# Kernel optimization log

Hardware: AMD Instinct MI355X
Metric: run time of the kernel (lower is better)

## Reference

```python
import jax, jax.numpy as jnp
import numpy as np

B = 256
NUM_PRIMARY = 32      # cfg.num_primary_caps
PRIM_ATOMS = 8
NUM_CLASSES = 10
DIGIT_ATOMS = 16
NUM_ROUTING = 3       # cfg.num_routing (DigitCap)
IN_DIM = 6 * 6 * NUM_PRIMARY  # 1152
NUM_PIXELS = 28 * 28 * 1


def squash(s, axis):
    # v = ||s||^2/(1+||s||^2) * s/||s||
    n2 = jnp.sum(jnp.square(s), axis=axis, keepdims=True)
    return s * (n2 / (1.0 + n2)) / jnp.sqrt(n2 + 1e-9)


def conv2d(x, w, stride):
    return jax.lax.conv_general_dilated(
        x, w, (stride, stride), 'VALID',
        dimension_numbers=('NCHW', 'OIHW', 'NCHW'))


def setup_inputs() -> dict:
    key = jax.random.key(0)
    ks = jax.random.split(key, 10)
    x = jax.random.uniform(ks[0], (B, 1, 28, 28), jnp.float32)
    labels = jax.random.randint(ks[1], (B,), 0, NUM_CLASSES)
    y = jax.nn.one_hot(labels, NUM_CLASSES, dtype=jnp.float32)
    conv1_w = 0.05 * jax.random.normal(ks[2], (256, 1, 9, 9), jnp.float32)
    conv1_b = jnp.full((256,), 0.1, jnp.float32)
    # primary capsule conv: 256 -> 32 caps * 8 atoms, k=9, s=2 (bias applied after routing)
    prim_w = 0.05 * jax.random.normal(ks[3], (NUM_PRIMARY * PRIM_ATOMS, 256, 9, 9), jnp.float32)
    prim_b = jnp.full((NUM_PRIMARY, PRIM_ATOMS), 0.1, jnp.float32)
    # digit capsule transform: [in_dim, in_atoms, out_dim, out_atoms]
    digit_w = 0.05 * jax.random.normal(ks[4], (IN_DIM, PRIM_ATOMS, NUM_CLASSES, DIGIT_ATOMS), jnp.float32)
    digit_b = jnp.full((NUM_CLASSES, DIGIT_ATOMS), 0.1, jnp.float32)
    w1 = 0.05 * jax.random.normal(ks[5], (NUM_CLASSES * DIGIT_ATOMS, 512), jnp.float32)
    b1 = jnp.zeros((512,), jnp.float32)
    w2 = 0.05 * jax.random.normal(ks[6], (512, 1024), jnp.float32)
    b2 = jnp.zeros((1024,), jnp.float32)
    w3 = 0.05 * jax.random.normal(ks[7], (1024, NUM_PIXELS), jnp.float32)
    b3 = jnp.zeros((NUM_PIXELS,), jnp.float32)
    return dict(x=x, y=y, conv1_w=conv1_w, conv1_b=conv1_b, prim_w=prim_w,
                prim_b=prim_b, digit_w=digit_w, digit_b=digit_b,
                w1=w1, b1=b1, w2=w2, b2=b2, w3=w3, b3=b3)


def reference(x, y, conv1_w, conv1_b, prim_w, prim_b, digit_w, digit_b,
              w1, b1, w2, b2, w3, b3):
    # conv stem
    h = jax.nn.relu(conv2d(x, conv1_w, 1) + conv1_b[None, :, None, None])  # [B,256,20,20]

    # PrimaryCap: conv votes [B, in_dim=1, out=32, atoms=8, 6, 6]; num_routing=1
    votes_p = conv2d(h, prim_w, 2).reshape(B, NUM_PRIMARY, PRIM_ATOMS, 6, 6)
    # one routing iter, input_dim=1: softmax(zeros) over output_dim -> uniform 1/32
    preact_p = votes_p / NUM_PRIMARY + prim_b[None, :, :, None, None]
    caps1 = squash(preact_p, axis=2)  # [B,32,8,6,6]

    # permute(0,1,3,4,2) then flatten -> [B, 1152, 8]
    x3 = jnp.transpose(caps1, (0, 1, 3, 4, 2)).reshape(B, IN_DIM, PRIM_ATOMS)

    # DigitCap votes: [B, in_dim, out_dim, out_atoms]
    votes = jnp.einsum('bia,iaot->biot', x3, digit_w)
    logits = jnp.zeros((B, IN_DIM, NUM_CLASSES), votes.dtype)
    act = None
    for _ in range(NUM_ROUTING):
        route = jax.nn.softmax(logits, axis=2)  # over output capsules
        preact = jnp.einsum('bio,biot->bot', route, votes) + digit_b
        act = squash(preact, axis=-1)  # [B,10,16]
        logits = logits + jnp.einsum('biot,bot->bio', votes, act)
    digit = act

    # Reconstruction: mask by label, 160 -> 512 -> 1024 -> 784
    masked = (digit * y[:, :, None]).reshape(B, NUM_CLASSES * DIGIT_ATOMS)
    r = jax.nn.relu(masked @ w1 + b1)
    r = jax.nn.relu(r @ w2 + b2)
    recon = jax.nn.sigmoid(r @ w3 + b3)
    return digit, recon
```

## Files before the change

### kernel.cpp

```cpp
#include <hip/hip_runtime.h>
#include <hip/hip_bf16.h>

typedef unsigned short u16;
typedef unsigned int u32;

static __device__ __forceinline__ float us2f(u16 u) {
    return __uint_as_float(((u32)u) << 16);
}
static __device__ __forceinline__ u16 f2bu(float f) {
    u32 u = __float_as_uint(f);
    return (u16)((u + 0x7fffu + ((u >> 16) & 1u)) >> 16);
}

typedef __attribute__((ext_vector_type(8))) __bf16 bf16x8;
typedef __attribute__((ext_vector_type(4))) float f32x4;

static __device__ __forceinline__ void async16(const u16* g, u16* l) {
    __builtin_amdgcn_global_load_lds(
        (const __attribute__((address_space(1))) unsigned int*)g,
        (__attribute__((address_space(3))) unsigned int*)l, 16, 0, 0);
}

__global__ void fill_sentinel(float* out, int n, float val) {
    int g = blockIdx.x * 256 + threadIdx.x;
    if (g < n) out[g] = val;
}

__global__ __launch_bounds__(256) void prep1(const float* __restrict__ pw,
    u16* __restrict__ wt, float* __restrict__ x3m)
{
    __shared__ u16 wl[81 * 258];
    const int bid = blockIdx.x, tid = threadIdx.x;
    if (bid < 256) {
        const float* ws = pw + (size_t)bid * 20736;
        for (int idx = tid; idx < 20736; idx += 256) {
            const int cc = idx / 81, kk = idx - cc * 81;
            wl[kk * 258 + cc] = f2bu(ws[idx]);
        }
        __syncthreads();
        u16* wo = wt + (size_t)bid * 20736;
        for (int q = tid; q < 20736; q += 256)
            wo[q] = wl[(q >> 8) * 258 + (q & 255)];
    } else {
        float4 z = {0.f, 0.f, 0.f, 0.f};
        reinterpret_cast<float4*>(x3m)[(size_t)(bid - 256) * 256 + tid] = z;
    }
}

__global__ __launch_bounds__(256) void prep2(const float* __restrict__ dw,
    u16* __restrict__ dwb_t, float* __restrict__ preactD)
{
    const int bid = blockIdx.x, tid = threadIdx.x;
    if (bid < 5760) {
        const int g = bid * 256 + tid;
        dwb_t[g] = f2bu(dw[g]);
    } else {
        float4 z = {0.f, 0.f, 0.f, 0.f};
        reinterpret_cast<float4*>(preactD)[(size_t)(bid - 5760) * 256 + tid] = z;
    }
}

__global__ __launch_bounds__(256) void conv1_kernel(const float* __restrict__ x,
    const float* __restrict__ wfull, const float* __restrict__ bias, u16* __restrict__ h)
{
    __shared__ float xs[784];
    __shared__ u16 wl[81 * 256];
    const int b = blockIdx.x >> 2, g = blockIdx.x & 3;
    const int c = threadIdx.x;
    for (int idx = c; idx < 784; idx += 256) xs[idx] = x[b * 784 + idx];
    for (int idx = c; idx < 20736; idx += 256)
        wl[idx] = f2bu(wfull[(idx & 255) * 81 + (idx >> 8)]);
    __syncthreads();
    const float bv = bias[c];
    #pragma unroll 1
    for (int iy = g * 5; iy < g * 5 + 5; ++iy) {
        float acc[20];
        #pragma unroll
        for (int i = 0; i < 20; ++i) acc[i] = bv;
        #pragma unroll 1
        for (int dy = 0; dy < 9; ++dy) {
            float xr[28];
            const float4* xrow = reinterpret_cast<const float4*>(&xs[(iy + dy) * 28]);
            #pragma unroll
            for (int i = 0; i < 7; ++i) {
                float4 v = xrow[i];
                xr[4*i] = v.x; xr[4*i+1] = v.y; xr[4*i+2] = v.z; xr[4*i+3] = v.w;
            }
            #pragma unroll
            for (int dx = 0; dx < 9; ++dx) {
                const float wv = us2f(wl[(dy * 9 + dx) * 256 + c]);
                #pragma unroll
                for (int ix = 0; ix < 20; ++ix) acc[ix] += xr[ix + dx] * wv;
            }
        }
        u16* hp = h + ((b * 20 + iy) * 20) * 256 + c;
        #pragma unroll
        for (int ix = 0; ix < 20; ++ix) hp[ix * 256] = f2bu(fmaxf(acc[ix], 0.f));
    }
}

__global__ __launch_bounds__(256, 2) void prim_gemm_split(const u16* __restrict__ h,
    const u16* __restrict__ wT, float* __restrict__ pm)
{
    __shared__ u16 As[3 * 4096];
    __shared__ u16 Bs[3 * 8192];
    const int tid = threadIdx.x;
    const int split = blockIdx.y;
    const int mBase = blockIdx.x * 128;
    const int lane = tid & 63, wv = tid >> 6;
    const int swzq = (tid & 3) ^ ((lane >> 3) & 3);
    const int rA = wv * 32 + (lane >> 2);
    const int rB = wv * 64 + (lane >> 2);
    int mA0 = mBase + rA;
    int bA0 = mA0 / 36, rr0 = mA0 % 36;
    const int aBase0 = ((bA0 * 20 + 2 * (rr0 / 6)) * 20 + 2 * (rr0 % 6)) * 256 + swzq * 8;
    int mA1 = mA0 + 16;
    int bA1 = mA1 / 36, rr1 = mA1 % 36;
    const int aBase1 = ((bA1 * 20 + 2 * (rr1 / 6)) * 20 + 2 * (rr1 % 6)) * 256 + swzq * 8;
    const u16* bp0 = wT + (size_t)rB * 20736 + swzq * 8;

    int kglob = split * 3456;
    int ky = kglob / 2304; int krem = kglob - ky * 2304;
    int kx = krem >> 8; int c0 = krem & 255;

    f32x4 acc[4][8];
    #pragma unroll
    for (int i = 0; i < 4; ++i)
        #pragma unroll
        for (int j = 0; j < 8; ++j) acc[i][j] = (f32x4){0.f, 0.f, 0.f, 0.f};

    const int wm = wv >> 1, wn = wv & 1;
    const int lcol = lane & 15, lquad = lane >> 4;
    const int rswz = (lquad ^ ((lcol >> 1) & 3)) * 8;
    const u16* Arow = As + (wm * 64 + lcol) * 32 + rswz;
    const u16* Brow = Bs + (wn * 128 + lcol) * 32 + rswz;
    u16* aD = As + wv * 1024;
    u16* bD = Bs + wv * 2048;

    #define STAGE(sel)  do {                                                   \
        const int koffA = (ky * 20 + kx) * 256 + c0;                           \
        async16(h + aBase0 + koffA, aD + (sel) * 4096);                        \
        async16(h + aBase1 + koffA, aD + (sel) * 4096 + 512);                  \
        async16(bp0 + kglob,          bD + (sel) * 8192);                      \
        async16(bp0 + 331776 + kglob, bD + (sel) * 8192 + 512);               \
        async16(bp0 + 663552 + kglob, bD + (sel) * 8192 + 1024);              \
        async16(bp0 + 995328 + kglob, bD + (sel) * 8192 + 1536);              \
        kglob += 32; c0 += 32;                                                 \
        if (c0 == 256) { c0 = 0; if (++kx == 9) { kx = 0; ++ky; } }            \
    } while (0)

    #define COMPUTE(sel)  do {                                                 \
        const u16* Ab = Arow + (sel) * 4096;                                   \
        const u16* Bb = Brow + (sel) * 8192;                                   \
        bf16x8 af[4], bfr[8];                                                  \
        _Pragma("unroll")                                                      \
        for (int i = 0; i < 4; ++i)                                            \
            af[i] = *reinterpret_cast<const bf16x8*>(Ab + i * 512);            \
        _Pragma("unroll")                                                      \
        for (int j = 0; j < 8; ++j)                                            \
            bfr[j] = *reinterpret_cast<const bf16x8*>(Bb + j * 512);           \
        __builtin_amdgcn_s_setprio(1);                                         \
        _Pragma("unroll")                                                      \
        for (int i = 0; i < 4; ++i)                                            \
            _Pragma("unroll")                                                  \
            for (int j = 0; j < 8; ++j)                                        \
                acc[i][j] = __builtin_amdgcn_mfma_f32_16x16x32_bf16(af[i], bfr[j], acc[i][j], 0, 0, 0); \
        __builtin_amdgcn_s_setprio(0);                                         \
    } while (0)

    STAGE(0);
    STAGE(1);
    int cb = 0, sb = 2;
    #pragma unroll 1
    for (int kt = 0; kt < 106; ++kt) {
        STAGE(sb);
        asm volatile("s_waitcnt vmcnt(12)" ::: "memory");
        __builtin_amdgcn_s_barrier();
        __builtin_amdgcn_sched_barrier(0);
        COMPUTE(cb);
        __builtin_amdgcn_sched_barrier(0);
        __builtin_amdgcn_s_barrier();
        __builtin_amdgcn_sched_barrier(0);
        cb = (cb == 2) ? 0 : cb + 1;
        sb = (sb == 2) ? 0 : sb + 1;
    }
    asm volatile("s_waitcnt vmcnt(6)" ::: "memory");
    __builtin_amdgcn_s_barrier();
    __builtin_amdgcn_sched_barrier(0);
    COMPUTE(1);
    __builtin_amdgcn_sched_barrier(0);
    asm volatile("s_waitcnt vmcnt(0)" ::: "memory");
    __builtin_amdgcn_s_barrier();
    __builtin_amdgcn_sched_barrier(0);
    COMPUTE(2);
    #undef STAGE
    #undef COMPUTE

    #pragma unroll
    for (int i = 0; i < 4; ++i) {
        const int mrow = mBase + wm * 64 + i * 16 + lquad * 4;
        #pragma unroll
        for (int j = 0; j < 8; ++j) {
            const int ncol = wn * 128 + j * 16 + lcol;
            #pragma unroll
            for (int r = 0; r < 4; ++r)
                unsafeAtomicAdd(&pm[(size_t)(mrow + r) * 256 + ncol], acc[i][j][r]);
        }
    }
}

__global__ __launch_bounds__(192) void votes_gemm(const float* __restrict__ x3m,
    const float* __restrict__ pb, const u16* __restrict__ dwb_t,
    u16* __restrict__ votes, int hb)
{
    __shared__ float dws[8 * 1280];
    __shared__ float x3s[64 * 64];
    __shared__ float pbs[256];
    const int ic = blockIdx.x * 8, bc = blockIdx.y * 64;
    const int tid = threadIdx.x;
    for (int q = tid; q < 256; q += 192) pbs[q] = pb[q];
    for (int q = tid; q < 10240; q += 192)
        dws[q] = us2f(dwb_t[(size_t)ic * 1280 + q]);
    __syncthreads();
    for (int g = tid; g < 512; g += 192) {
        const int b_l = g >> 3, i_l = g & 7;
        const int i = ic + i_l, cap = i / 36, p = i - cap * 36;
        const float* src = &x3m[((size_t)(hb + bc + b_l) * 36 + p) * 256 + cap * 8];
        float v[8]; float n2 = 0.f;
        #pragma unroll
        for (int a = 0; a < 8; ++a) {
            v[a] = src[a] * (1.f / 32.f) + pbs[cap * 8 + a];
            n2 += v[a] * v[a];
        }
        const float scale = (n2 / (1.f + n2)) * rsqrtf(n2 + 1e-9f);
        #pragma unroll
        for (int a = 0; a < 8; ++a)
            x3s[b_l * 64 + i_l * 8 + a] = v[a] * scale;
    }
    __syncthreads();
    if (tid < 160) {
        const int ot = tid;
        float dwr[8][8];
        #pragma unroll
        for (int i_l = 0; i_l < 8; ++i_l)
            #pragma unroll
            for (int a = 0; a < 8; ++a)
                dwr[i_l][a] = dws[i_l * 1280 + a * 160 + ot];
        #pragma unroll 1
        for (int b_l = 0; b_l < 64; ++b_l) {
            u16 ob[8];
            #pragma unroll
            for (int i_l = 0; i_l < 8; ++i_l) {
                const float* xp = &x3s[b_l * 64 + i_l * 8];
                float v = 0.f;
                #pragma unroll
                for (int a = 0; a < 8; ++a) v += xp[a] * dwr[i_l][a];
                ob[i_l] = f2bu(v);
            }
            uint4 o4;
            o4.x = (u32)ob[0] | ((u32)ob[1] << 16);
            o4.y = (u32)ob[2] | ((u32)ob[3] << 16);
            o4.z = (u32)ob[4] | ((u32)ob[5] << 16);
            o4.w = (u32)ob[6] | ((u32)ob[7] << 16);
            *reinterpret_cast<uint4*>(&votes[((size_t)(bc + b_l) * 160 + ot) * 1152 + ic]) = o4;
        }
    }
}

__global__ __launch_bounds__(256) void routing_fused(const u16* __restrict__ votes,
    const float* __restrict__ pD_prev, const float* __restrict__ db,
    float* __restrict__ logits, float* __restrict__ pD_next, int hb, int mode)
{
    __shared__ u16 vs16[160 * 146];
    __shared__ float route_s[144 * 10];
    __shared__ float act_s[160];
    const int ic = blockIdx.x * 144, b_l = blockIdx.y, gb = hb + b_l;
    const int tid = threadIdx.x;

    for (int q = tid; q < 2880; q += 256) {
        const int ot = q / 18, ch = q - ot * 18;
        const uint4 d = *reinterpret_cast<const uint4*>(
            &votes[((size_t)b_l * 160 + ot) * 1152 + ic + ch * 8]);
        u32* vp = reinterpret_cast<u32*>(&vs16[ot * 146 + ch * 8]);
        vp[0] = d.x; vp[1] = d.y; vp[2] = d.z; vp[3] = d.w;
    }
    if (mode >= 1 && tid < 160) {
        float pre = pD_prev[(size_t)gb * 160 + tid] + db[tid];
        float sq = pre * pre;
        sq += __shfl_xor(sq, 1); sq += __shfl_xor(sq, 2);
        sq += __shfl_xor(sq, 4); sq += __shfl_xor(sq, 8);
        act_s[tid] = pre * (sq / (1.f + sq)) * rsqrtf(sq + 1e-9f);
    }
    __syncthreads();

    if (mode >= 1) {
        if (tid < 144) {
            float acc[10];
            #pragma unroll
            for (int k = 0; k < 10; ++k) acc[k] = 0.f;
            #pragma unroll 4
            for (int ot = 0; ot < 160; ++ot)
                acc[ot >> 4] += us2f(vs16[ot * 146 + tid]) * act_s[ot];
            float* lp = &logits[((size_t)gb * 1152 + ic + tid) * 10];
            float l[10];
            if (mode == 1) {
                #pragma unroll
                for (int k = 0; k < 10; ++k) { l[k] = acc[k]; lp[k] = l[k]; }
            } else {
                #pragma unroll
                for (int k = 0; k < 10; ++k) { l[k] = lp[k] + acc[k]; lp[k] = l[k]; }
            }
            float mx = -1e30f;
            #pragma unroll
            for (int k = 0; k < 10; ++k) mx = fmaxf(mx, l[k]);
            float s = 0.f;
            #pragma unroll
            for (int k = 0; k < 10; ++k) { l[k] = __expf(l[k] - mx); s += l[k]; }
            const float inv = 1.f / s;
            #pragma unroll
            for (int k = 0; k < 10; ++k) route_s[tid * 10 + k] = l[k] * inv;
        }
        __syncthreads();
    }

    if (tid < 160) {
        const int o = tid >> 4;
        const u16* vrow = &vs16[tid * 146];
        float acc2 = 0.f;
        if (mode == 0) {
            float s = 0.f;
            #pragma unroll 8
            for (int i = 0; i < 144; ++i) s += us2f(vrow[i]);
            acc2 = 0.1f * s;
        } else {
            const float* rp = &route_s[o];
            #pragma unroll 8
            for (int i = 0; i < 144; ++i)
                acc2 += rp[i * 10] * us2f(vrow[i]);
        }
        unsafeAtomicAdd(&pD_next[(size_t)gb * 160 + tid], acc2);
    }
}

__global__ __launch_bounds__(256) void mlp_layer(const float* __restrict__ in,
    const float* __restrict__ maskY, const float* __restrict__ w,
    const float* __restrict__ bias, float* __restrict__ outp, int K, int N, int mode,
    const float* __restrict__ db2, float* __restrict__ dout)
{
    __shared__ float ins[4 * 1024];
    __shared__ float scl[40];
    const int b0 = blockIdx.x * 4;
    const int n = blockIdx.y * 256 + threadIdx.x;
    if (db2) {
        if (threadIdx.x < 40) {
            const int b_l = threadIdx.x / 10, o = threadIdx.x - b_l * 10;
            const float* pp = &in[(size_t)(b0 + b_l) * 160 + o * 16];
            float n2 = 0.f;
            #pragma unroll
            for (int t = 0; t < 16; ++t) {
                float pv = pp[t] + db2[o * 16 + t];
                n2 += pv * pv;
            }
            scl[threadIdx.x] = (n2 / (1.f + n2)) * rsqrtf(n2 + 1e-9f);
        }
        __syncthreads();
        for (int idx = threadIdx.x; idx < 4 * 160; idx += 256) {
            const int b_l = idx / 160, j = idx - b_l * 160;
            float a = (in[(size_t)(b0 + b_l) * 160 + j] + db2[j]) * scl[b_l * 10 + (j >> 4)];
            if (blockIdx.y == 0 && dout) dout[(size_t)(b0 + b_l) * 160 + j] = a;
            ins[idx] = a * maskY[(b0 + b_l) * 10 + (j >> 4)];
        }
    } else {
        for (int idx = threadIdx.x; idx < 4 * K; idx += 256) {
            float v = in[(size_t)b0 * K + idx];
            if (maskY) {
                const int b_l = idx / K, j = idx % K;
                v *= maskY[(b0 + b_l) * 10 + (j >> 4)];
            }
            ins[idx] = v;
        }
    }
    __syncthreads();
    if (n < N) {
        float a0 = 0.f, a1 = 0.f, a2 = 0.f, a3 = 0.f;
        for (int k = 0; k < K; ++k) {
            const float wvv = w[(size_t)k * N + n];
            a0 += ins[k] * wvv;
            a1 += ins[K + k] * wvv;
            a2 += ins[2 * K + k] * wvv;
            a3 += ins[3 * K + k] * wvv;
        }
        const float bv = bias[n];
        float v[4] = {a0 + bv, a1 + bv, a2 + bv, a3 + bv};
        #pragma unroll
        for (int j = 0; j < 4; ++j) {
            float xv = v[j];
            xv = (mode == 0) ? fmaxf(xv, 0.f) : 1.f / (1.f + __expf(-xv));
            outp[(size_t)(b0 + j) * N + n] = xv;
        }
    }
}

extern "C" void kernel_launch(void* const* d_in, const int* in_sizes, int n_in,
                              void* d_out, int out_size, void* d_ws, size_t ws_size,
                              hipStream_t stream) {
    const float* x   = (const float*)d_in[0];
    const float* y   = (const float*)d_in[1];
    const float* c1w = (const float*)d_in[2];
    const float* c1b = (const float*)d_in[3];
    const float* pw  = (const float*)d_in[4];
    const float* pb  = (const float*)d_in[5];
    const float* dw  = (const float*)d_in[6];
    const float* db  = (const float*)d_in[7];
    const float* w1  = (const float*)d_in[8];
    const float* b1  = (const float*)d_in[9];
    const float* w2  = (const float*)d_in[10];
    const float* b2  = (const float*)d_in[11];
    const float* w3  = (const float*)d_in[12];
    const float* b3  = (const float*)d_in[13];
    float* out = (float*)d_out;
    char* ws = (char*)d_ws;

    static const int exp_sizes[14] = {200704, 2560, 20736, 256, 5308416, 256,
                                      1474560, 160, 81920, 512, 524288, 1024,
                                      802816, 784};
    int bad = (n_in == 14) ? -1 : -2;
    if (bad == -1)
        for (int i = 0; i < 14; ++i) if (in_sizes[i] != exp_sizes[i]) { bad = i; break; }
    if (bad != -1) {
        fill_sentinel<<<(out_size + 255) / 256, 256, 0, stream>>>(out, out_size,
            7168.f + 16.f * (float)(bad + 1));
        return;
    }
    const size_t NEEDED = 72482816ULL;
    if (ws_size < NEEDED) {
        fill_sentinel<<<(out_size + 255) / 256, 256, 0, stream>>>(out, out_size, 111.0f);
        return;
    }

    u16*   h       = (u16*)(ws);
    u16*   wT2     = (u16*)(ws + 52428800);
    float* x3m     = (float*)(ws + 63045632);
    u16*   votes   = (u16*)(ws);
    float* logits  = (float*)(ws + 47185920);
    float* preactD = (float*)(ws + 59146240);
    u16*   dwb_t   = (u16*)(ws + 59637760);
    float* r1      = (float*)(ws + 62586880);
    float* r2      = (float*)(ws + 63111168);

    prep1<<<2560, 256, 0, stream>>>(pw, wT2, x3m);
    conv1_kernel<<<1024, 256, 0, stream>>>(x, c1w, c1b, h);
    prim_gemm_split<<<dim3(72, 6), 256, 0, stream>>>(h, wT2, x3m);
    prep2<<<5880, 256, 0, stream>>>(dw, dwb_t, preactD);

    float* pD0 = preactD, *pD1 = preactD + 40960, *pD2 = preactD + 81920;
    for (int half = 0; half < 2; ++half) {
        const int hb = half * 128;
        votes_gemm<<<dim3(144, 2), 192, 0, stream>>>(x3m, pb, dwb_t, votes, hb);
        routing_fused<<<dim3(8, 128), 256, 0, stream>>>(votes, pD0, db, logits, pD0, hb, 0);
        routing_fused<<<dim3(8, 128), 256, 0, stream>>>(votes, pD0, db, logits, pD1, hb, 1);
        routing_fused<<<dim3(8, 128), 256, 0, stream>>>(votes, pD1, db, logits, pD2, hb, 2);
    }

    mlp_layer<<<dim3(64, 2), 256, 0, stream>>>(pD2, y, w1, b1, r1, 160, 512, 0, db, out);
    mlp_layer<<<dim3(64, 4), 256, 0, stream>>>(r1, (float*)nullptr, w2, b2, r2, 512, 1024, 0,
                                               (const float*)nullptr, (float*)nullptr);
    mlp_layer<<<dim3(64, 4), 256, 0, stream>>>(r2, (float*)nullptr, w3, b3, out + 40960, 1024, 784, 1,
                                               (const float*)nullptr, (float*)nullptr);
}
```

Baseline: 753.0 us.

## Rewrite conv1 as MFMA implicit GEMM with split-bf16 input

Replaces the scalar per-channel conv1 loop with an implicit-GEMM kernel on 16x16x32 bf16 MFMA. The 81 taps are padded to K=96, and the input is gathered from LDS and split into hi/lo bf16 parts to keep accuracy close to fp32. The conv1 weights are pre-converted to a padded bf16 layout in prep1, stored in the tail of the x3m buffer. That tail is zeroed with a memset before the primary GEMM accumulates into it. The aim is to remove the scalar FMA cost of the stem conv, at the price of two MFMAs per tile and scattered bf16 stores of h.

```diff
diff --git a/kernel.cpp b/kernel.cpp
--- a/kernel.cpp
+++ b/kernel.cpp
@@ -27,7 +27,8 @@
 }
 
 __global__ __launch_bounds__(256) void prep1(const float* __restrict__ pw,
-    u16* __restrict__ wt, float* __restrict__ x3m)
+    u16* __restrict__ wt, float* __restrict__ x3m,
+    const float* __restrict__ c1w, u16* __restrict__ wc1b)
 {
     __shared__ u16 wl[81 * 258];
     const int bid = blockIdx.x, tid = threadIdx.x;
@@ -41,9 +42,16 @@
         u16* wo = wt + (size_t)bid * 20736;
         for (int q = tid; q < 20736; q += 256)
             wo[q] = wl[(q >> 8) * 258 + (q & 255)];
-    } else {
+    } else if (bid < 2548) {
         float4 z = {0.f, 0.f, 0.f, 0.f};
         reinterpret_cast<float4*>(x3m)[(size_t)(bid - 256) * 256 + tid] = z;
+    } else {
+        for (int idx = tid; idx < 24576; idx += 256) {
+            const int s = idx >> 13, rem = idx & 8191;
+            const int n = rem >> 5, kk = rem & 31;
+            const int k = s * 32 + kk;
+            wc1b[idx] = (k < 81) ? f2bu(c1w[n * 81 + k]) : (u16)0;
+        }
     }
 }
 
@@ -60,42 +68,89 @@
     }
 }
 
-__global__ __launch_bounds__(256) void conv1_kernel(const float* __restrict__ x,
-    const float* __restrict__ wfull, const float* __restrict__ bias, u16* __restrict__ h)
-{
-    __shared__ float xs[784];
-    __shared__ u16 wl[81 * 256];
-    const int b = blockIdx.x >> 2, g = blockIdx.x & 3;
-    const int c = threadIdx.x;
-    for (int idx = c; idx < 784; idx += 256) xs[idx] = x[b * 784 + idx];
-    for (int idx = c; idx < 20736; idx += 256)
-        wl[idx] = f2bu(wfull[(idx & 255) * 81 + (idx >> 8)]);
+__global__ __launch_bounds__(256, 2) void conv1_mfma(const float* __restrict__ x,
+    const u16* __restrict__ wc1b, const float* __restrict__ bias, u16* __restrict__ h)
+{
+    __shared__ float xs[1568];
+    const int tid = threadIdx.x;
+    const int mBase = blockIdx.x * 128;
+    const int b0 = mBase / 400;
+    const int lane = tid & 63, wv = tid >> 6;
+    const int wm = wv >> 1, wn = wv & 1;
+    const int lcol = lane & 15, lquad = lane >> 4;
+
+    {
+        const int b1 = (b0 + 1 < 256) ? b0 + 1 : b0;
+        for (int i = tid; i < 784; i += 256) {
+            xs[i] = x[b0 * 784 + i];
+            xs[784 + i] = x[b1 * 784 + i];
+        }
+    }
     __syncthreads();
-    const float bv = bias[c];
+
+    float bj[8];
+    #pragma unroll
+    for (int j = 0; j < 8; ++j) bj[j] = bias[wn * 128 + j * 16 + lcol];
+
+    int xbase[4];
+    #pragma unroll
+    for (int i = 0; i < 4; ++i) {
+        const int m = mBase + wm * 64 + i * 16 + lcol;
+        const int img = (m / 400) - b0;
+        const int rr = m % 400;
+        const int iy = rr / 20, ix = rr - iy * 20;
+        xbase[i] = img * 784 + iy * 28 + ix;
+    }
+
+    f32x4 acc[4][8];
+    #pragma unroll
+    for (int i = 0; i < 4; ++i)
+        #pragma unroll
+        for (int j = 0; j < 8; ++j) acc[i][j] = (f32x4){0.f, 0.f, 0.f, 0.f};
+
     #pragma unroll 1
-    for (int iy = g * 5; iy < g * 5 + 5; ++iy) {
-        float acc[20];
-        #pragma unroll
-        for (int i = 0; i < 20; ++i) acc[i] = bv;
-        #pragma unroll 1
-        for (int dy = 0; dy < 9; ++dy) {
-            float xr[28];
-            const float4* xrow = reinterpret_cast<const float4*>(&xs[(iy + dy) * 28]);
-            #pragma unroll
-            for (int i = 0; i < 7; ++i) {
-                float4 v = xrow[i];
-                xr[4*i] = v.x; xr[4*i+1] = v.y; xr[4*i+2] = v.z; xr[4*i+3] = v.w;
+    for (int s = 0; s < 3; ++s) {
+        bf16x8 bfr[8];
+        const u16* bp = wc1b + s * 8192 + (wn * 128 + lcol) * 32 + lquad * 8;
+        #pragma unroll
+        for (int j = 0; j < 8; ++j)
+            bfr[j] = *reinterpret_cast<const bf16x8*>(bp + j * 512);
+
+        bf16x8 ah[4], al[4];
+        #pragma unroll
+        for (int i = 0; i < 4; ++i) {
+            union { bf16x8 v; u16 u[8]; } H, L;
+            #pragma unroll
+            for (int e = 0; e < 8; ++e) {
+                int k = s * 32 + lquad * 8 + e;
+                if (k > 80) k = 0;
+                const int dy = k / 9, dx = k - dy * 9;
+                const float xv = xs[xbase[i] + dy * 28 + dx];
+                const u16 hu = f2bu(xv);
+                H.u[e] = hu;
+                L.u[e] = f2bu(xv - us2f(hu));
             }
-            #pragma unroll
-            for (int dx = 0; dx < 9; ++dx) {
-                const float wv = us2f(wl[(dy * 9 + dx) * 256 + c]);
-                #pragma unroll
-                for (int ix = 0; ix < 20; ++ix) acc[ix] += xr[ix + dx] * wv;
+            ah[i] = H.v; al[i] = L.v;
+        }
+        #pragma unroll
+        for (int i = 0; i < 4; ++i)
+            #pragma unroll
+            for (int j = 0; j < 8; ++j) {
+                acc[i][j] = __builtin_amdgcn_mfma_f32_16x16x32_bf16(ah[i], bfr[j], acc[i][j], 0, 0, 0);
+                acc[i][j] = __builtin_amdgcn_mfma_f32_16x16x32_bf16(al[i], bfr[j], acc[i][j], 0, 0, 0);
             }
-        }
-        u16* hp = h + ((b * 20 + iy) * 20) * 256 + c;
-        #pragma unroll
-        for (int ix = 0; ix < 20; ++ix) hp[ix * 256] = f2bu(fmaxf(acc[ix], 0.f));
+    }
+
+    #pragma unroll
+    for (int i = 0; i < 4; ++i) {
+        const int mrow = mBase + wm * 64 + i * 16 + lquad * 4;
+        #pragma unroll
+        for (int j = 0; j < 8; ++j) {
+            const int ncol = wn * 128 + j * 16 + lcol;
+            #pragma unroll
+            for (int r = 0; r < 4; ++r)
+                h[(size_t)(mrow + r) * 256 + ncol] = f2bu(fmaxf(acc[i][j][r] + bj[j], 0.f));
+        }
     }
 }
 
@@ -441,6 +496,7 @@
     u16*   h       = (u16*)(ws);
     u16*   wT2     = (u16*)(ws + 52428800);
     float* x3m     = (float*)(ws + 63045632);
+    u16*   wc1b    = (u16*)(ws + 72433664);
     u16*   votes   = (u16*)(ws);
     float* logits  = (float*)(ws + 47185920);
     float* preactD = (float*)(ws + 59146240);
@@ -448,8 +504,9 @@
     float* r1      = (float*)(ws + 62586880);
     float* r2      = (float*)(ws + 63111168);
 
-    prep1<<<2560, 256, 0, stream>>>(pw, wT2, x3m);
-    conv1_kernel<<<1024, 256, 0, stream>>>(x, c1w, c1b, h);
+    prep1<<<2549, 256, 0, stream>>>(pw, wT2, x3m, c1w, wc1b);
+    conv1_mfma<<<800, 256, 0, stream>>>(x, wc1b, c1b, h);
+    hipMemsetAsync(wc1b, 0, 49152, stream);
     prim_gemm_split<<<dim3(72, 6), 256, 0, stream>>>(h, wT2, x3m);
     prep2<<<5880, 256, 0, stream>>>(dw, dwb_t, preactD);
 
```

New measurement: 720.1 us. -4.4%, faster.
